# Kernel tuning notes

Hardware: AMD Instinct MI355X
Metric: run time of the kernel (lower is better)

The kernel has to match this reference:

```python
import jax, jax.numpy as jnp
import numpy as np

NUM_FEATURES = 256
NUM_PIDS = 5532
NUM_CQ = 5000
OIM_SCALAR = 30.0
IGNORE_INDEX = 5554  # roi_label 5555 -> label 5554 -> ignored by cross_entropy
N = 8192
UNLABELED_FRAC = 0.3


def _l2norm(x):
    return x / jnp.linalg.norm(x, axis=-1, keepdims=True)


def setup_inputs() -> dict:
    key = jax.random.key(0)
    k1, k2, k3, k4, k5 = jax.random.split(key, 5)
    inputs = _l2norm(jax.random.normal(k1, (N, NUM_FEATURES), dtype=jnp.float32))
    # roi_label values are 1..num_pids for labeled persons, 5555 for unlabeled;
    # all >= 1 so the `label >= 0` filter in the torch module keeps every row
    # (keeps shapes static / jit-friendly while matching the math exactly).
    labels = jax.random.randint(k2, (N,), 1, NUM_PIDS + 1, dtype=jnp.int32)
    unlabeled = jax.random.uniform(k3, (N,)) < UNLABELED_FRAC
    roi_label = jnp.where(unlabeled, IGNORE_INDEX + 1, labels).astype(jnp.int32)
    lut = _l2norm(jax.random.normal(k4, (NUM_PIDS, NUM_FEATURES), dtype=jnp.float32))
    cq = _l2norm(jax.random.normal(k5, (NUM_CQ, NUM_FEATURES), dtype=jnp.float32))
    return {"inputs": inputs, "roi_label": roi_label, "lut": lut, "cq": cq}


def reference(inputs, roi_label, lut, cq):
    # targets = cat(roi_label); label = targets - 1; inds = label >= 0 keeps all rows here
    label = roi_label - 1  # [N], values in [0, NUM_PIDS-1] or IGNORE_INDEX
    # OIMSMR.forward: projected = [inputs @ lut.T | inputs @ cq.T]
    logits = jnp.concatenate([inputs @ lut.T, inputs @ cq.T], axis=1)  # [N, P+Q]
    logits = logits * OIM_SCALAR
    # cross_entropy with ignore_index=5554 (mean over non-ignored samples)
    valid = label != IGNORE_INDEX
    safe_label = jnp.clip(label, 0, logits.shape[1] - 1)
    logp = jax.nn.log_softmax(logits, axis=1)  # [N, P+Q]
    nll = -jnp.take_along_axis(logp, safe_label[:, None], axis=1)[:, 0]  # [N]
    n_valid = jnp.maximum(jnp.sum(valid.astype(jnp.float32)), 1.0)
    loss = jnp.sum(jnp.where(valid, nll, 0.0)) / n_valid
    return loss
```

## Files before the change

kernel.cpp:

```cpp
#include <hip/hip_runtime.h>
#include <hip/hip_bf16.h>
#include <cstdint>
#include <cstddef>

#define N_ROWS 8192
#define K_DIM  256
#define NP     5532
#define NC     10532
#define NCPAD  10752
#define IGN    5554
#define BM     128
#define BN     128
#define BK     64
#define CT     84
#define NBLK   (CT * 64)
#define CPX    (NBLK / 8)

using f32x4 = __attribute__((ext_vector_type(4))) float;
using i64x2 = __attribute__((ext_vector_type(2))) long;

__global__ __launch_bounds__(256) void oim_convert(
    const float* __restrict__ X, const float* __restrict__ lut,
    const float* __restrict__ cq,
    unsigned char* __restrict__ Xb, unsigned char* __restrict__ Wb)
{
    const int XCH = (N_ROWS * K_DIM) / 8;
    const int WCH = (NCPAD * K_DIM) / 8;
    int c = blockIdx.x * 256 + threadIdx.x;
    if (c >= XCH + WCH) return;
    const float* src = nullptr;
    unsigned char* dst;
    int row, qg;
    if (c < XCH) {
        row = c >> 5; qg = c & 31;
        src = X + (size_t)c * 8;
        dst = Xb + (size_t)row * K_DIM;
    } else {
        int wc = c - XCH;
        row = wc >> 5; qg = wc & 31;
        dst = Wb + (size_t)row * K_DIM;
        if (row < NP)      src = lut + (size_t)row * K_DIM + qg * 8;
        else if (row < NC) src = cq + (size_t)(row - NP) * K_DIM + qg * 8;
    }
    dst += (qg >> 3) * 64 + (qg & 3) * 16 + ((qg >> 2) & 1) * 8;
    unsigned int lo = 0, hi = 0;
    if (src) {
        float4 v0 = *reinterpret_cast<const float4*>(src);
        float4 v1 = *reinterpret_cast<const float4*>(src + 4);
        lo = __builtin_amdgcn_cvt_pk_fp8_f32(v0.x, v0.y, 0,  false);
        lo = __builtin_amdgcn_cvt_pk_fp8_f32(v0.z, v0.w, lo, true);
        hi = __builtin_amdgcn_cvt_pk_fp8_f32(v1.x, v1.y, 0,  false);
        hi = __builtin_amdgcn_cvt_pk_fp8_f32(v1.z, v1.w, hi, true);
    }
    uint2 o; o.x = lo; o.y = hi;
    *reinterpret_cast<uint2*>(dst) = o;
}

__global__ __launch_bounds__(256, 4) void oim_gemm(
    const unsigned char* __restrict__ Xb, const unsigned char* __restrict__ Wb,
    const int* __restrict__ roi,
    float* __restrict__ partial, float* __restrict__ labelLogit)
{
    const int bid = blockIdx.x;
    const int L   = (bid & 7) * CPX + (bid >> 3);
    const int ct  = L >> 6;
    const int rt  = L & 63;
    const int row0 = rt * BM;
    const int col0 = ct * BN;
    const int tid  = threadIdx.x;
    const int wave = tid >> 6;
    const int lane = tid & 63;
    const int wm   = (wave >> 1) * 64;
    const int wn   = (wave & 1) * 64;

    __shared__ __align__(16) unsigned char As[BM * BK];
    __shared__ __align__(16) unsigned char Bs[BN * BK];
    __shared__ int   lbl[BM];
    __shared__ float rs[BM][2];

    if (tid < BM) lbl[tid] = roi[row0 + tid] - 1;

    const unsigned char* aP[2];
    const unsigned char* bP[2];
#pragma unroll
    for (int i = 0; i < 2; ++i) {
        int c  = i * 256 + tid;
        int r  = ((c >> 3) << 1) | ((c >> 2) & 1);
        int gq = (c & 3) ^ ((c >> 3) & 3);
        aP[i] = Xb + (size_t)(row0 + r) * K_DIM + gq * 16;
        bP[i] = Wb + (size_t)(col0 + r) * K_DIM + gq * 16;
    }

    const int rA = wm + (lane & 15);
    const int rB = wn + (lane & 15);
    const int gK = lane >> 4;
    const int aOff = ((rA >> 1) << 7) + ((rA & 1) << 6)
                   + ((gK ^ ((rA >> 1) & 3)) << 4);
    const int bOff = ((rB >> 1) << 7) + ((rB & 1) << 6)
                   + ((gK ^ ((rB >> 1) & 3)) << 4);

    f32x4 acc[4][4] = {};
    long av0[4], av1[4], bv0[4], bv1[4];

    auto ldsread = [&]() {
#pragma unroll
        for (int m = 0; m < 4; ++m) {
            i64x2 v = *reinterpret_cast<const i64x2*>(As + aOff + m * 1024);
            av0[m] = v.x; av1[m] = v.y;
        }
#pragma unroll
        for (int n = 0; n < 4; ++n) {
            i64x2 v = *reinterpret_cast<const i64x2*>(Bs + bOff + n * 1024);
            bv0[n] = v.x; bv1[n] = v.y;
        }
    };
    auto mfma = [&]() {
#pragma unroll
        for (int m = 0; m < 4; ++m)
#pragma unroll
            for (int n = 0; n < 4; ++n)
                acc[m][n] = __builtin_amdgcn_mfma_f32_16x16x32_fp8_fp8(
                    av0[m], bv0[n], acc[m][n], 0, 0, 0);
#pragma unroll
        for (int m = 0; m < 4; ++m)
#pragma unroll
            for (int n = 0; n < 4; ++n)
                acc[m][n] = __builtin_amdgcn_mfma_f32_16x16x32_fp8_fp8(
                    av1[m], bv1[n], acc[m][n], 0, 0, 0);
    };

#define STAGE(T)                                                              \
    do {                                                                      \
        __builtin_amdgcn_global_load_lds(                                     \
            (const __attribute__((address_space(1))) void*)aP[0],             \
            (__attribute__((address_space(3))) void*)                         \
                ((char*)As + wave * 1024), 16, (T) * 64, 0);                  \
        __builtin_amdgcn_global_load_lds(                                     \
            (const __attribute__((address_space(1))) void*)aP[1],             \
            (__attribute__((address_space(3))) void*)                         \
                ((char*)As + 4096 + wave * 1024), 16, (T) * 64, 0);           \
        __builtin_amdgcn_global_load_lds(                                     \
            (const __attribute__((address_space(1))) void*)bP[0],             \
            (__attribute__((address_space(3))) void*)                         \
                ((char*)Bs + wave * 1024), 16, (T) * 64, 0);                  \
        __builtin_amdgcn_global_load_lds(                                     \
            (const __attribute__((address_space(1))) void*)bP[1],             \
            (__attribute__((address_space(3))) void*)                         \
                ((char*)Bs + 4096 + wave * 1024), 16, (T) * 64, 0);           \
    } while (0)

#define ITER(T)                                                               \
    do {                                                                      \
        ldsread();                                                            \
        __syncthreads();       \
        STAGE((T) + 1);        \
        mfma();                \
        __syncthreads();       \
    } while (0)

    STAGE(0);
    __syncthreads();
    ITER(0); ITER(1); ITER(2);
    ldsread();
    mfma();
#undef ITER
#undef STAGE

#pragma unroll
    for (int m = 0; m < 4; ++m) {
#pragma unroll
        for (int reg = 0; reg < 4; ++reg) {
            int lrow = wm + m * 16 + (lane >> 4) * 4 + reg;
            int grow = row0 + lrow;
            int lab  = lbl[lrow];
            float s = 0.0f;
#pragma unroll
            for (int n = 0; n < 4; ++n) {
                int gcol = col0 + wn + n * 16 + (lane & 15);
                float logit = acc[m][n][reg] * 30.0f;
                s += __expf(logit - 30.0f);
                if (gcol == lab) labelLogit[grow] = logit;
            }
#pragma unroll
            for (int off = 1; off < 16; off <<= 1) s += __shfl_xor(s, off, 64);
            if ((lane & 15) == 0) rs[lrow][wave & 1] = s;
        }
    }
    __syncthreads();
    if (tid < BM)
        partial[(size_t)ct * N_ROWS + row0 + tid] = rs[tid][0] + rs[tid][1];
}

__global__ __launch_bounds__(256) void oim_rownll(
    const float* __restrict__ partial, const float* __restrict__ labelLogit,
    const int* __restrict__ roi, float* __restrict__ blksum)
{
    __shared__ float s1[256], s2[256];
    int tid = threadIdx.x;
    int r = blockIdx.x * 256 + tid;
    float S = 0.0f;
    for (int t = 0; t < CT; ++t) S += partial[(size_t)t * N_ROWS + r];
    float lse = 30.0f + logf(S);
    int lab = roi[r] - 1;
    bool valid = (lab != IGN);
    s1[tid] = valid ? (lse - labelLogit[r]) : 0.0f;
    s2[tid] = valid ? 1.0f : 0.0f;
    __syncthreads();
    for (int o = 128; o > 0; o >>= 1) {
        if (tid < o) { s1[tid] += s1[tid + o]; s2[tid] += s2[tid + o]; }
        __syncthreads();
    }
    if (tid == 0) {
        blksum[blockIdx.x]      = s1[0];
        blksum[32 + blockIdx.x] = s2[0];
    }
}

__global__ __launch_bounds__(64) void oim_reduce(
    const float* __restrict__ blksum, float* __restrict__ out)
{
    int tid = threadIdx.x;
    float a = (tid < 32) ? blksum[tid]      : 0.0f;
    float b = (tid < 32) ? blksum[32 + tid] : 0.0f;
#pragma unroll
    for (int off = 32; off > 0; off >>= 1) {
        a += __shfl_xor(a, off, 64);
        b += __shfl_xor(b, off, 64);
    }
    if (tid == 0) out[0] = a / fmaxf(b, 1.0f);
}

extern "C" void kernel_launch(void* const* d_in, const int* in_sizes, int n_in,
                              void* d_out, int out_size, void* d_ws, size_t ws_size,
                              hipStream_t stream)
{
    const float* X   = (const float*)d_in[0];
    const int*   roi = (const int*)  d_in[1];
    const float* lut = (const float*)d_in[2];
    const float* cq  = (const float*)d_in[3];
    float* out = (float*)d_out;

    char* ws = (char*)d_ws;
    unsigned char* Xb = (unsigned char*)ws;
    unsigned char* Wb = Xb + (size_t)N_ROWS * K_DIM;
    float* partial    = (float*)(Wb + (size_t)NCPAD * K_DIM);
    float* labelLogit = partial + (size_t)CT * N_ROWS;
    float* blksum     = labelLogit + N_ROWS;
    size_t need = (size_t)N_ROWS * K_DIM + (size_t)NCPAD * K_DIM
                + (size_t)CT * N_ROWS * 4 + (size_t)(N_ROWS + 64) * 4;
    if (ws_size < need) return;

    const int TOT_CHUNKS = ((N_ROWS + NCPAD) * K_DIM) / 8;
    oim_convert<<<(TOT_CHUNKS + 255) / 256, 256, 0, stream>>>(X, lut, cq, Xb, Wb);
    oim_gemm<<<NBLK, 256, 0, stream>>>(Xb, Wb, roi, partial, labelLogit);
    oim_rownll<<<N_ROWS / 256, 256, 0, stream>>>(partial, labelLogit, roi, blksum);
    oim_reduce<<<1, 64, 0, stream>>>(blksum, out);
}
```

Before: 65.24 us.

## Double K tile to 128 and cut barrier rounds in FP8 GEMM

Raises the K tile from 64 to 128 so the 256-deep reduction runs in two LDS stages instead of four, halving the number of barrier pairs and global-to-LDS rounds. LDS layout and swizzle are rewritten to 128-byte rows with an XOR over eight 16-byte groups, and fragments are read in two K-halves per stage. LDS per block doubles and the launch-bounds occupancy hint drops from 4 to 3 blocks per CU, which reduces latency hiding across blocks.

```diff
diff --git a/kernel.cpp b/kernel.cpp
--- a/kernel.cpp
+++ b/kernel.cpp
@@ -11,7 +11,7 @@
 #define IGN    5554
 #define BM     128
 #define BN     128
-#define BK     64
+#define BK     128
 #define CT     84
 #define NBLK   (CT * 64)
 #define CPX    (NBLK / 8)
@@ -56,7 +56,7 @@
     *reinterpret_cast<uint2*>(dst) = o;
 }
 
-__global__ __launch_bounds__(256, 4) void oim_gemm(
+__global__ __launch_bounds__(256, 3) void oim_gemm(
     const unsigned char* __restrict__ Xb, const unsigned char* __restrict__ Wb,
     const int* __restrict__ roi,
     float* __restrict__ partial, float* __restrict__ labelLogit)
@@ -80,90 +80,85 @@
 
     if (tid < BM) lbl[tid] = roi[row0 + tid] - 1;
 
-    const unsigned char* aP[2];
-    const unsigned char* bP[2];
-#pragma unroll
-    for (int i = 0; i < 2; ++i) {
-        int c  = i * 256 + tid;
-        int r  = ((c >> 3) << 1) | ((c >> 2) & 1);
-        int gq = (c & 3) ^ ((c >> 3) & 3);
-        aP[i] = Xb + (size_t)(row0 + r) * K_DIM + gq * 16;
-        bP[i] = Wb + (size_t)(col0 + r) * K_DIM + gq * 16;
+    const unsigned char* aP[4];
+    const unsigned char* bP[4];
+#pragma unroll
+    for (int i = 0; i < 4; ++i) {
+        int c = i * 256 + tid;
+        int r = c >> 3;
+        int u = c & 7;
+        int s = ((u ^ (r & 7)) << 4);
+        aP[i] = Xb + (size_t)(row0 + r) * K_DIM + s;
+        bP[i] = Wb + (size_t)(col0 + r) * K_DIM + s;
     }
 
     const int rA = wm + (lane & 15);
     const int rB = wn + (lane & 15);
-    const int gK = lane >> 4;
-    const int aOff = ((rA >> 1) << 7) + ((rA & 1) << 6)
-                   + ((gK ^ ((rA >> 1) & 3)) << 4);
-    const int bOff = ((rB >> 1) << 7) + ((rB & 1) << 6)
-                   + ((gK ^ ((rB >> 1) & 3)) << 4);
+    const int gs = lane >> 4;
+    int aO[2], bO[2];
+#pragma unroll
+    for (int kb = 0; kb < 2; ++kb) {
+        aO[kb] = rA * 128 + (((kb * 4 + gs) ^ (rA & 7)) << 4);
+        bO[kb] = rB * 128 + (((kb * 4 + gs) ^ (rB & 7)) << 4);
+    }
 
     f32x4 acc[4][4] = {};
-    long av0[4], av1[4], bv0[4], bv1[4];
-
-    auto ldsread = [&]() {
+    long xa0[4], xa1[4], xb0[4], xb1[4];
+
+    auto readfrag = [&](int kb) {
 #pragma unroll
         for (int m = 0; m < 4; ++m) {
-            i64x2 v = *reinterpret_cast<const i64x2*>(As + aOff + m * 1024);
-            av0[m] = v.x; av1[m] = v.y;
+            i64x2 v = *reinterpret_cast<const i64x2*>(As + aO[kb] + m * 2048);
+            xa0[m] = v.x; xa1[m] = v.y;
         }
 #pragma unroll
         for (int n = 0; n < 4; ++n) {
-            i64x2 v = *reinterpret_cast<const i64x2*>(Bs + bOff + n * 1024);
-            bv0[n] = v.x; bv1[n] = v.y;
+            i64x2 v = *reinterpret_cast<const i64x2*>(Bs + bO[kb] + n * 2048);
+            xb0[n] = v.x; xb1[n] = v.y;
         }
     };
-    auto mfma = [&]() {
+    auto mfmafrag = [&]() {
 #pragma unroll
         for (int m = 0; m < 4; ++m)
 #pragma unroll
             for (int n = 0; n < 4; ++n)
                 acc[m][n] = __builtin_amdgcn_mfma_f32_16x16x32_fp8_fp8(
-                    av0[m], bv0[n], acc[m][n], 0, 0, 0);
+                    xa0[m], xb0[n], acc[m][n], 0, 0, 0);
 #pragma unroll
         for (int m = 0; m < 4; ++m)
 #pragma unroll
             for (int n = 0; n < 4; ++n)
                 acc[m][n] = __builtin_amdgcn_mfma_f32_16x16x32_fp8_fp8(
-                    av1[m], bv1[n], acc[m][n], 0, 0, 0);
+                    xa1[m], xb1[n], acc[m][n], 0, 0, 0);
     };
 
 #define STAGE(T)                                                              \
     do {                                                                      \
-        __builtin_amdgcn_global_load_lds(                                     \
-            (const __attribute__((address_space(1))) void*)aP[0],             \
-            (__attribute__((address_space(3))) void*)                         \
-                ((char*)As + wave * 1024), 16, (T) * 64, 0);                  \
-        __builtin_amdgcn_global_load_lds(                                     \
-            (const __attribute__((address_space(1))) void*)aP[1],             \
-            (__attribute__((address_space(3))) void*)                         \
-                ((char*)As + 4096 + wave * 1024), 16, (T) * 64, 0);           \
-        __builtin_amdgcn_global_load_lds(                                     \
-            (const __attribute__((address_space(1))) void*)bP[0],             \
-            (__attribute__((address_space(3))) void*)                         \
-                ((char*)Bs + wave * 1024), 16, (T) * 64, 0);                  \
-        __builtin_amdgcn_global_load_lds(                                     \
-            (const __attribute__((address_space(1))) void*)bP[1],             \
-            (__attribute__((address_space(3))) void*)                         \
-                ((char*)Bs + 4096 + wave * 1024), 16, (T) * 64, 0);           \
+        _Pragma("unroll")                                                     \
+        for (int i = 0; i < 4; ++i) {                                         \
+            __builtin_amdgcn_global_load_lds(                                 \
+                (const __attribute__((address_space(1))) void*)aP[i],         \
+                (__attribute__((address_space(3))) void*)                     \
+                    ((char*)As + i * 4096 + wave * 1024), 16, (T) * 128, 0);  \
+            __builtin_amdgcn_global_load_lds(                                 \
+                (const __attribute__((address_space(1))) void*)bP[i],         \
+                (__attribute__((address_space(3))) void*)                     \
+                    ((char*)Bs + i * 4096 + wave * 1024), 16, (T) * 128, 0);  \
+        }                                                                     \
     } while (0)
 
-#define ITER(T)                                                               \
-    do {                                                                      \
-        ldsread();                                                            \
-        __syncthreads();       \
-        STAGE((T) + 1);        \
-        mfma();                \
-        __syncthreads();       \
-    } while (0)
-
     STAGE(0);
     __syncthreads();
-    ITER(0); ITER(1); ITER(2);
-    ldsread();
-    mfma();
-#undef ITER
+
+    readfrag(0); mfmafrag();
+    readfrag(1);
+    __syncthreads();
+    STAGE(1);
+    mfmafrag();
+    __syncthreads();
+
+    readfrag(0); mfmafrag();
+    readfrag(1); mfmafrag();
 #undef STAGE
 
 #pragma unroll
```

After: 64.18 us. No clear change (-1.6%).
